# Kernel tuning notes

Measured on AMD Instinct MI355X. Metric: run time of the kernel, lower is better.

The kernel has to match this reference:

```python
import jax, jax.numpy as jnp
import numpy as np

N, C, H, W = 2048, 16, 32, 32
E = 16384


def _conv(x, w, b):
    # 3x3 conv, stride 1, padding 1, NCHW/OIHW
    y = jax.lax.conv_general_dilated(
        x, w, window_strides=(1, 1), padding=((1, 1), (1, 1)),
        dimension_numbers=('NCHW', 'OIHW', 'NCHW'))
    return y + b[None, :, None, None]


def _get_nodes(fv, edges, positive):
    # fv: [N,C,H,W]; edges: [E,3] = (a, rel, b)
    rel = edges[:, 1]
    m = (rel > 0) if positive else (rel < 0)
    wmask = m.astype(fv.dtype)[:, None, None, None]  # [E,1,1,1]
    a = edges[:, 0]
    b = edges[:, 2]
    # symmetric scatter_add: fv[a] -> b and fv[b] -> a (masked edges contribute 0)
    nodes = jnp.zeros_like(fv)
    nodes = nodes.at[b].add(fv[a] * wmask)
    nodes = nodes.at[a].add(fv[b] * wmask)
    return nodes


def setup_inputs() -> dict:
    key = jax.random.key(0)
    ks = jax.random.split(key, 10)
    x = jax.random.normal(ks[0], (N, C, H, W), dtype=jnp.float32)
    ids = jax.random.randint(ks[1], (E, 2), 0, N)
    rel = jnp.where(jax.random.bernoulli(ks[2], 0.5, (E,)), 1, -1).astype(jnp.int64)
    edges = jnp.stack([ids[:, 0].astype(jnp.int64), rel, ids[:, 1].astype(jnp.int64)], axis=1)
    s = 0.05
    w1 = jax.random.normal(ks[3], (32, 48, 3, 3), dtype=jnp.float32) * s
    b1 = jax.random.normal(ks[4], (32,), dtype=jnp.float32) * s
    w2 = jax.random.normal(ks[5], (32, 32, 3, 3), dtype=jnp.float32) * s
    b2 = jax.random.normal(ks[6], (32,), dtype=jnp.float32) * s
    w3 = jax.random.normal(ks[7], (16, 32, 3, 3), dtype=jnp.float32) * s
    b3 = jax.random.normal(ks[8], (16,), dtype=jnp.float32) * s
    return {"x": x, "edges": edges, "w1": w1, "b1": b1, "w2": w2, "b2": b2, "w3": w3, "b3": b3}


def reference(x, edges, w1, b1, w2, b2, w3, b3):
    neigh = _get_nodes(x, edges, True)
    non_neigh = _get_nodes(x, edges, False)
    enc = jnp.concatenate([x, neigh, non_neigh], axis=1)  # [N,48,H,W]
    h = _conv(enc, w1, b1)
    h = _conv(h, w2, b2)
    return _conv(h, w3, b3)  # [N,16,H,W]
```

## Files before the change

kernel.cpp:

```cpp
#include <hip/hip_runtime.h>


#define NNODES 2048
#define HW 1024
#define PLANE 16384
#define CAP 128
#define SLICE_PX 32
#define NSLICE 32
#define NPB 8

typedef float v4f __attribute__((ext_vector_type(4)));
typedef short v8s __attribute__((ext_vector_type(8)));
typedef unsigned int v4u __attribute__((ext_vector_type(4)));

__device__ inline unsigned short f2bfu(float f) {
    unsigned u = __float_as_uint(f);
    u += 0x7fffu + ((u >> 16) & 1u);
    return (unsigned short)(u >> 16);
}
__device__ inline unsigned pk2(float a, float b) {
    return (unsigned)f2bfu(a) | ((unsigned)f2bfu(b) << 16);
}
__device__ inline void add2(float& a, float& b, unsigned u) {
    a += __uint_as_float(u << 16);
    b += __uint_as_float(u & 0xffff0000u);
}

__global__ __launch_bounds__(256) void build_lists(
    const int* __restrict__ edges, int E, int* __restrict__ cnt, int* __restrict__ lists)
{
    int e = blockIdx.x * 256 + threadIdx.x;
    if (e >= E) return;
    int a = edges[3 * e + 0];
    int rel = edges[3 * e + 1];
    int b = edges[3 * e + 2];
    int s = (rel > 0) ? 0 : 1;
    int slot = atomicAdd(&cnt[b * 2 + s], 1);
    if (slot < CAP) lists[((size_t)(b * 2 + s)) * CAP + slot] = a;
    slot = atomicAdd(&cnt[a * 2 + s], 1);
    if (slot < CAP) lists[((size_t)(a * 2 + s)) * CAP + slot] = b;
}

__global__ __launch_bounds__(256) void xpose_bf16(
    const float* __restrict__ x, ushort* __restrict__ xb)
{
    int n = blockIdx.x, t = threadIdx.x;
    const float4* src = (const float4*)(x + (size_t)n * PLANE);
    float vv[64];
#pragma unroll
    for (int i = 0; i < 16; i++) {
        float4 v = src[i * 256 + t];
        vv[i * 4 + 0] = v.x; vv[i * 4 + 1] = v.y; vv[i * 4 + 2] = v.z; vv[i * 4 + 3] = v.w;
    }
    uint4* dst = (uint4*)(xb + (size_t)n * HW * 16);
#pragma unroll
    for (int j = 0; j < 4; j++) {
        uint4 o0, o1;
        o0.x = pk2(vv[0 * 4 + j], vv[1 * 4 + j]);
        o0.y = pk2(vv[2 * 4 + j], vv[3 * 4 + j]);
        o0.z = pk2(vv[4 * 4 + j], vv[5 * 4 + j]);
        o0.w = pk2(vv[6 * 4 + j], vv[7 * 4 + j]);
        o1.x = pk2(vv[8 * 4 + j], vv[9 * 4 + j]);
        o1.y = pk2(vv[10 * 4 + j], vv[11 * 4 + j]);
        o1.z = pk2(vv[12 * 4 + j], vv[13 * 4 + j]);
        o1.w = pk2(vv[14 * 4 + j], vv[15 * 4 + j]);
        dst[(4 * t + j) * 2 + 0] = o0;
        dst[(4 * t + j) * 2 + 1] = o1;
    }
}

#define ACC16(P0, P1) do { \
    add2(acc[0],  acc[1],  (P0).x); add2(acc[2],  acc[3],  (P0).y); \
    add2(acc[4],  acc[5],  (P0).z); add2(acc[6],  acc[7],  (P0).w); \
    add2(acc[8],  acc[9],  (P1).x); add2(acc[10], acc[11], (P1).y); \
    add2(acc[12], acc[13], (P1).z); add2(acc[14], acc[15], (P1).w); } while (0)

__global__ __launch_bounds__(256) void gather_enc_slice(
    const ushort* __restrict__ xb, const int* __restrict__ cnt,
    const int* __restrict__ lists, ushort* __restrict__ enc)
{
    int idx = blockIdx.x;
    int x8 = idx & 7;
    int g  = (idx >> 3) & 255;
    int p  = idx >> 11;
    int slice = p * 8 + x8;
    int t = threadIdx.x;
    int nodebase = g * NPB;
    int node = nodebase + (t >> 5);
    int px = slice * SLICE_PX + (t & 31);

    __shared__ int slist[NPB * 2 * CAP];
    __shared__ int sdeg[NPB * 2];
    {
        const uint4* lsrc = (const uint4*)(lists + (size_t)nodebase * 2 * CAP);
        uint4* ldst = (uint4*)slist;
        ldst[t] = lsrc[t];
        ldst[256 + t] = lsrc[256 + t];
        if (t < NPB * 2) sdeg[t] = min(cnt[nodebase * 2 + t], CAP);
    }
    __syncthreads();

    v4u* edst = (v4u*)(enc + ((size_t)node * HW + px) * 32);
#pragma unroll
    for (int s = 0; s < 2; s++) {
        const int lbase = ((t >> 5) * 2 + s) * CAP;
        const int d = sdeg[(t >> 5) * 2 + s];
        float acc[16];
#pragma unroll
        for (int i = 0; i < 16; i++) acc[i] = 0.f;
        v4u a0 = {0,0,0,0}, a1 = {0,0,0,0}, b0 = {0,0,0,0}, b1 = {0,0,0,0};
        if (d >= 1) {
            const v4u* sp = (const v4u*)(xb + ((size_t)slist[lbase] * HW + px) * 16);
            a0 = sp[0]; a1 = sp[1];
        }
        if (d >= 2) {
            const v4u* sp = (const v4u*)(xb + ((size_t)slist[lbase + 1] * HW + px) * 16);
            b0 = sp[0]; b1 = sp[1];
        }
        for (int k = 2; k < d; k++) {
            const v4u* sp = (const v4u*)(xb + ((size_t)slist[lbase + k] * HW + px) * 16);
            v4u n0 = sp[0], n1 = sp[1];
            ACC16(a0, a1);
            a0 = b0; a1 = b1; b0 = n0; b1 = n1;
        }
        if (d >= 1) { ACC16(a0, a1); ACC16(b0, b1); }

        v4u o0, o1;
        o0.x = pk2(acc[0],  acc[1]);  o0.y = pk2(acc[2],  acc[3]);
        o0.z = pk2(acc[4],  acc[5]);  o0.w = pk2(acc[6],  acc[7]);
        o1.x = pk2(acc[8],  acc[9]);  o1.y = pk2(acc[10], acc[11]);
        o1.z = pk2(acc[12], acc[13]); o1.w = pk2(acc[14], acc[15]);
        __builtin_nontemporal_store(o0, edst + s * 2 + 0);
        __builtin_nontemporal_store(o1, edst + s * 2 + 1);
    }
}

template<int CI_REAL, int KCH, int CO>
__global__ __launch_bounds__(256) void prep_wfrag(
    const float* __restrict__ wt, ushort* __restrict__ wf)
{
    const int total = (CO / 16) * 9 * KCH * 64;
    for (int idx = blockIdx.x * 256 + threadIdx.x; idx < total; idx += gridDim.x * 256) {
        int lane = idx & 63;
        int t = idx >> 6;
        int kc = t % KCH; t /= KCH;
        int khw = t % 9;  t /= 9;
        int cot = t;
        int nco = cot * 16 + (lane & 15);
        int kq  = lane >> 4;
        float w[8];
#pragma unroll
        for (int j = 0; j < 8; j++) {
            int k = kc * 32 + kq * 8 + j;
            w[j] = (k < CI_REAL) ? wt[((size_t)nco * CI_REAL + k) * 9 + khw] : 0.f;
        }
        uint4 o;
        o.x = pk2(w[0], w[1]); o.y = pk2(w[2], w[3]);
        o.z = pk2(w[4], w[5]); o.w = pk2(w[6], w[7]);
        *(uint4*)&wf[(size_t)idx * 8] = o;
    }
}

template<int CI_REAL, int CIP_G, int CIP_L, int KCH, int CO, bool OUT_F32, bool SPLIT>
__global__ __launch_bounds__(256) void conv_mfma(
    const ushort* __restrict__ in, const ushort* __restrict__ in2,
    const ushort* __restrict__ wf, const float* __restrict__ bias,
    ushort* __restrict__ outb, float* __restrict__ outf)
{
    __shared__ ushort tile[320 * CIP_L + 8];
    const int n = blockIdx.x >> 2;
    const int r0 = (blockIdx.x & 3) * 8;
    const int CH4 = CIP_G / 8;
    const int CH4_1 = SPLIT ? (CH4 - 2) : CH4;

    const uint4* gsrc  = (const uint4*)(in + (size_t)n * HW * (CH4_1 * 8));
    const uint4* gsrc2 = SPLIT ? (const uint4*)(in2 + (size_t)n * HW * 16) : nullptr;
    for (int idx = threadIdx.x; idx < 320 * CH4; idx += 256) {
        int lp = idx / CH4;
        int ch = idx - lp * CH4;
        int gr = r0 - 1 + (lp >> 5);
        uint4 val = make_uint4(0, 0, 0, 0);
        if (gr >= 0 && gr < 32) {
            size_t gpx = (size_t)(gr * 32 + (lp & 31));
            if (SPLIT && ch < 2) val = gsrc2[gpx * 2 + ch];
            else                 val = gsrc[gpx * CH4_1 + (SPLIT ? ch - 2 : ch)];
        }
        *(uint4*)&tile[lp * CIP_L + ch * 8] = val;
    }
    __syncthreads();

    const int wv = threadIdx.x >> 6;
    const int lane = threadIdx.x & 63;
    const int l15 = lane & 15;
    const int kq = lane >> 4;

    const int cotile = (CO == 32) ? (wv >> 1) : 0;
    const int cob = cotile * 16;
    const int nco = cob + l15;

    const v8s* wfv = (const v8s*)wf;
    v8s bfrag[9 * KCH];
#pragma unroll
    for (int khw = 0; khw < 9; khw++)
#pragma unroll
        for (int kc = 0; kc < KCH; kc++)
            bfrag[khw * KCH + kc] = wfv[(size_t)(((cotile * 9 + khw) * KCH + kc) * 64 + lane)];
    const float bv = bias[nco];

    int mt0, mtstep, nmt;
    if (CO == 32) { mt0 = wv & 1; mtstep = 2; nmt = 8; }
    else          { mt0 = wv;     mtstep = 4; nmt = 4; }

    for (int it = 0; it < nmt; it++) {
        int mtile = mt0 + it * mtstep;
        int r = r0 + (mtile >> 1);
        int c = (mtile & 1) * 16 + l15;
        v4f acc = {bv, bv, bv, bv};
#pragma unroll
        for (int khw = 0; khw < 9; khw++) {
            int dh = khw / 3 - 1, dw = (khw % 3) - 1;
            int rr = r + dh;
            if (rr < 0 || rr > 31) continue;
            int cc = c + dw;
            bool okc = (cc >= 0) && (cc <= 31);
            int lp = (rr - r0 + 1) * 32 + (okc ? cc : 0);
#pragma unroll
            for (int kc = 0; kc < KCH; kc++) {
                v8s a = *(const v8s*)&tile[lp * CIP_L + kc * 32 + kq * 8];
                bool kok = (kc * 32 + 32 <= CI_REAL) || (kc * 32 + kq * 8 < CI_REAL);
                if (!okc || !kok) a = (v8s)0;
                acc = __builtin_amdgcn_mfma_f32_16x16x32_bf16(a, bfrag[khw * KCH + kc], acc, 0, 0, 0);
            }
        }
        int pbase = r * 32 + (mtile & 1) * 16 + kq * 4;
        if (OUT_F32) {
            float4 o; o.x = acc[0]; o.y = acc[1]; o.z = acc[2]; o.w = acc[3];
            *(float4*)(outf + ((size_t)n * CO + nco) * HW + pbase) = o;
        } else {
#pragma unroll
            for (int reg = 0; reg < 4; reg++)
                outb[((size_t)n * HW + pbase + reg) * CO + nco] = (ushort)f2bfu(acc[reg]);
        }
    }
}

extern "C" void kernel_launch(void* const* d_in, const int* in_sizes, int n_in,
                              void* d_out, int out_size, void* d_ws, size_t ws_size,
                              hipStream_t stream)
{
    const float* x     = (const float*)d_in[0];
    const int*   edges = (const int*)d_in[1];
    const float* w1    = (const float*)d_in[2];
    const float* b1    = (const float*)d_in[3];
    const float* w2    = (const float*)d_in[4];
    const float* b2    = (const float*)d_in[5];
    const float* w3    = (const float*)d_in[6];
    const float* b3    = (const float*)d_in[7];
    float* out = (float*)d_out;

    const int E = in_sizes[1] / 3;

    ushort* enc = (ushort*)d_ws;
    ushort* h1  = enc + (size_t)NNODES * HW * 32;
    ushort* xb  = h1  + (size_t)NNODES * HW * 32;
    int*    cnt   = (int*)(xb + (size_t)NNODES * HW * 16);
    int*    lists = cnt + NNODES * 2;
    ushort* wf1 = (ushort*)(lists + (size_t)NNODES * 2 * CAP);
    ushort* wf2 = wf1 + 2 * 9 * 2 * 64 * 8;
    ushort* wf3 = wf2 + 2 * 9 * 1 * 64 * 8;
    ushort* h2  = enc;

    hipMemsetAsync(cnt, 0, NNODES * 2 * sizeof(int), stream);
    build_lists<<<(E + 255) / 256, 256, 0, stream>>>(edges, E, cnt, lists);

    prep_wfrag<48, 2, 32><<<9, 256, 0, stream>>>(w1, wf1);
    prep_wfrag<32, 1, 32><<<5, 256, 0, stream>>>(w2, wf2);
    prep_wfrag<32, 1, 16><<<3, 256, 0, stream>>>(w3, wf3);

    xpose_bf16<<<NNODES, 256, 0, stream>>>(x, xb);
    gather_enc_slice<<<NSLICE * (NNODES / NPB), 256, 0, stream>>>(xb, cnt, lists, enc);

    conv_mfma<48, 48, 56, 2, 32, false, true><<<NNODES * 4, 256, 0, stream>>>(enc, xb, wf1, b1, h1, nullptr);
    conv_mfma<32, 32, 40, 1, 32, false, false><<<NNODES * 4, 256, 0, stream>>>(h1, nullptr, wf2, b2, h2, nullptr);
    conv_mfma<32, 32, 40, 1, 16, true, false><<<NNODES * 4, 256, 0, stream>>>(h2, nullptr, wf3, b3, nullptr, out);
}
```

Baseline: 721.5 us.

## Pad conv LDS tile with zero halo and share A fragments across output-channel tiles

The shared-memory input tile now holds a 34-column zero-padded halo, so the inner MFMA loop needs no per-tap bounds checks or masking of A fragments. Each wave computes both 16-channel output tiles from a single A-fragment load, which halves LDS reads per MFMA and removes the duplicated spatial work split across waves. The M-tile loop is fully unrolled. In exchange, every wave holds both sets of weight fragments in registers, which raises VGPR pressure and may lower occupancy. The tile also grows slightly, and padding channels are loaded explicitly as zeros.

Result: slower. 792.4 us (+9.8%).

```diff
diff --git a/kernel.cpp b/kernel.cpp
--- a/kernel.cpp
+++ b/kernel.cpp
@@ -161,31 +161,38 @@
     }
 }
 
-template<int CI_REAL, int CIP_G, int CIP_L, int KCH, int CO, bool OUT_F32, bool SPLIT>
+template<int CI_REAL, int CIP_L, int CH4S, int KCH, int CO, bool OUT_F32, bool SPLIT>
 __global__ __launch_bounds__(256) void conv_mfma(
     const ushort* __restrict__ in, const ushort* __restrict__ in2,
     const ushort* __restrict__ wf, const float* __restrict__ bias,
     ushort* __restrict__ outb, float* __restrict__ outf)
 {
-    __shared__ ushort tile[320 * CIP_L + 8];
+    constexpr int NCOT = CO / 16;
+    __shared__ ushort tile[340 * CIP_L + 16];
     const int n = blockIdx.x >> 2;
     const int r0 = (blockIdx.x & 3) * 8;
-    const int CH4 = CIP_G / 8;
-    const int CH4_1 = SPLIT ? (CH4 - 2) : CH4;
-
-    const uint4* gsrc  = (const uint4*)(in + (size_t)n * HW * (CH4_1 * 8));
+
+    const uint4* gsrc  = (const uint4*)(in + (size_t)n * HW * 32);
     const uint4* gsrc2 = SPLIT ? (const uint4*)(in2 + (size_t)n * HW * 16) : nullptr;
-    for (int idx = threadIdx.x; idx < 320 * CH4; idx += 256) {
-        int lp = idx / CH4;
-        int ch = idx - lp * CH4;
-        int gr = r0 - 1 + (lp >> 5);
+    if (threadIdx.x < 16) tile[340 * CIP_L + threadIdx.x] = 0;
+    for (int idx = threadIdx.x; idx < 340 * CH4S; idx += 256) {
+        int p34 = idx / CH4S;
+        int ch  = idx - p34 * CH4S;
+        int row = p34 / 34;
+        int col = p34 - row * 34;
+        int gr = r0 - 1 + row;
+        int gc = col - 1;
         uint4 val = make_uint4(0, 0, 0, 0);
-        if (gr >= 0 && gr < 32) {
-            size_t gpx = (size_t)(gr * 32 + (lp & 31));
-            if (SPLIT && ch < 2) val = gsrc2[gpx * 2 + ch];
-            else                 val = gsrc[gpx * CH4_1 + (SPLIT ? ch - 2 : ch)];
-        }
-        *(uint4*)&tile[lp * CIP_L + ch * 8] = val;
+        if (gr >= 0 && gr < 32 && gc >= 0 && gc < 32) {
+            size_t gpx = (size_t)(gr * 32 + gc);
+            if (SPLIT) {
+                if (ch < 2)      val = gsrc2[gpx * 2 + ch];
+                else if (ch < 6) val = gsrc[gpx * 4 + ch - 2];
+            } else {
+                val = gsrc[gpx * CH4S + ch];
+            }
+        }
+        *(uint4*)&tile[p34 * CIP_L + ch * 8] = val;
     }
     __syncthreads();
 
@@ -194,52 +201,55 @@
     const int l15 = lane & 15;
     const int kq = lane >> 4;
 
-    const int cotile = (CO == 32) ? (wv >> 1) : 0;
-    const int cob = cotile * 16;
-    const int nco = cob + l15;
-
     const v8s* wfv = (const v8s*)wf;
-    v8s bfrag[9 * KCH];
-#pragma unroll
-    for (int khw = 0; khw < 9; khw++)
-#pragma unroll
-        for (int kc = 0; kc < KCH; kc++)
-            bfrag[khw * KCH + kc] = wfv[(size_t)(((cotile * 9 + khw) * KCH + kc) * 64 + lane)];
-    const float bv = bias[nco];
-
-    int mt0, mtstep, nmt;
-    if (CO == 32) { mt0 = wv & 1; mtstep = 2; nmt = 8; }
-    else          { mt0 = wv;     mtstep = 4; nmt = 4; }
-
-    for (int it = 0; it < nmt; it++) {
-        int mtile = mt0 + it * mtstep;
-        int r = r0 + (mtile >> 1);
-        int c = (mtile & 1) * 16 + l15;
-        v4f acc = {bv, bv, bv, bv};
+    v8s bfrag[NCOT][9 * KCH];
+#pragma unroll
+    for (int cot = 0; cot < NCOT; cot++)
+#pragma unroll
+        for (int khw = 0; khw < 9; khw++)
+#pragma unroll
+            for (int kc = 0; kc < KCH; kc++)
+                bfrag[cot][khw * KCH + kc] =
+                    wfv[(size_t)(((cot * 9 + khw) * KCH + kc) * 64 + lane)];
+    float bv[NCOT];
+#pragma unroll
+    for (int cot = 0; cot < NCOT; cot++) bv[cot] = bias[cot * 16 + l15];
+
+#pragma unroll
+    for (int it = 0; it < 4; it++) {
+        const int mtile = wv + it * 4;
+        const int rloc = mtile >> 1;
+        const int base = (rloc * 34 + (mtile & 1) * 16 + l15) * CIP_L + kq * 8;
+        v4f acc[NCOT];
+#pragma unroll
+        for (int cot = 0; cot < NCOT; cot++)
+            acc[cot] = (v4f){bv[cot], bv[cot], bv[cot], bv[cot]};
 #pragma unroll
         for (int khw = 0; khw < 9; khw++) {
-            int dh = khw / 3 - 1, dw = (khw % 3) - 1;
-            int rr = r + dh;
-            if (rr < 0 || rr > 31) continue;
-            int cc = c + dw;
-            bool okc = (cc >= 0) && (cc <= 31);
-            int lp = (rr - r0 + 1) * 32 + (okc ? cc : 0);
+            const int off = ((khw / 3) * 34 + (khw % 3)) * CIP_L;
 #pragma unroll
             for (int kc = 0; kc < KCH; kc++) {
-                v8s a = *(const v8s*)&tile[lp * CIP_L + kc * 32 + kq * 8];
-                bool kok = (kc * 32 + 32 <= CI_REAL) || (kc * 32 + kq * 8 < CI_REAL);
-                if (!okc || !kok) a = (v8s)0;
-                acc = __builtin_amdgcn_mfma_f32_16x16x32_bf16(a, bfrag[khw * KCH + kc], acc, 0, 0, 0);
+                v8s a = *(const v8s*)&tile[base + off + kc * 32];
+                acc[0] = __builtin_amdgcn_mfma_f32_16x16x32_bf16(
+                    a, bfrag[0][khw * KCH + kc], acc[0], 0, 0, 0);
+                if (NCOT > 1)
+                    acc[1] = __builtin_amdgcn_mfma_f32_16x16x32_bf16(
+                        a, bfrag[1][khw * KCH + kc], acc[1], 0, 0, 0);
             }
         }
-        int pbase = r * 32 + (mtile & 1) * 16 + kq * 4;
-        if (OUT_F32) {
-            float4 o; o.x = acc[0]; o.y = acc[1]; o.z = acc[2]; o.w = acc[3];
-            *(float4*)(outf + ((size_t)n * CO + nco) * HW + pbase) = o;
-        } else {
-#pragma unroll
-            for (int reg = 0; reg < 4; reg++)
-                outb[((size_t)n * HW + pbase + reg) * CO + nco] = (ushort)f2bfu(acc[reg]);
+        const int pbase = (r0 + rloc) * 32 + (mtile & 1) * 16 + kq * 4;
+#pragma unroll
+        for (int cot = 0; cot < NCOT; cot++) {
+            if (OUT_F32) {
+                float4 o;
+                o.x = acc[cot][0]; o.y = acc[cot][1]; o.z = acc[cot][2]; o.w = acc[cot][3];
+                *(float4*)(outf + ((size_t)n * CO + cot * 16 + l15) * HW + pbase) = o;
+            } else {
+#pragma unroll
+                for (int reg = 0; reg < 4; reg++)
+                    outb[((size_t)n * HW + pbase + reg) * CO + cot * 16 + l15] =
+                        (ushort)f2bfu(acc[cot][reg]);
+            }
         }
     }
 }
@@ -280,7 +290,10 @@
     xpose_bf16<<<NNODES, 256, 0, stream>>>(x, xb);
     gather_enc_slice<<<NSLICE * (NNODES / NPB), 256, 0, stream>>>(xb, cnt, lists, enc);
 
-    conv_mfma<48, 48, 56, 2, 32, false, true><<<NNODES * 4, 256, 0, stream>>>(enc, xb, wf1, b1, h1, nullptr);
-    conv_mfma<32, 32, 40, 1, 32, false, false><<<NNODES * 4, 256, 0, stream>>>(h1, nullptr, wf2, b2, h2, nullptr);
-    conv_mfma<32, 32, 40, 1, 16, true, false><<<NNODES * 4, 256, 0, stream>>>(h2, nullptr, wf3, b3, nullptr, out);
-}
+    conv_mfma<48, 56, 7, 2, 32, false, true><<<NNODES * 4, 256, 0, stream>>>(
+        enc, xb, wf1, b1, h1, nullptr);
+    conv_mfma<32, 40, 4, 1, 32, false, false><<<NNODES * 4, 256, 0, stream>>>(
+        h1, nullptr, wf2, b2, h2, nullptr);
+    conv_mfma<32, 40, 4, 1, 16, true, false><<<NNODES * 4, 256, 0, stream>>>(
+        h2, nullptr, wf3, b3, nullptr, out);
+}
```
